# Kernel tuning notes

Measured on AMD Instinct MI355X. Metric: run time of the kernel, lower is better.

Reference implementation:

```python
import jax, jax.numpy as jnp
import numpy as np

B, T, D = 2, 1024, 768
H, HS = 12, 64          # n_head, head_size = n_embed // n_head
E, K = 8, 1             # num_experts, top-k (MoeLayer default k=1)
DF = 4 * D              # FFN hidden
EPS = 1e-5


def _ln(x, g, b):
    mu = jnp.mean(x, axis=-1, keepdims=True)
    var = jnp.mean(jnp.square(x - mu), axis=-1, keepdims=True)
    return (x - mu) * jax.lax.rsqrt(var + EPS) * g + b


def setup_inputs() -> dict:
    key = jax.random.key(0)
    ks = jax.random.split(key, 12)
    s = 0.02
    return {
        "x": jax.random.normal(ks[0], (B, T, D), dtype=jnp.float32),
        "ln1_g": jnp.ones((D,), jnp.float32),
        "ln1_b": jnp.zeros((D,), jnp.float32),
        "ln2_g": jnp.ones((D,), jnp.float32),
        "ln2_b": jnp.zeros((D,), jnp.float32),
        "Wq": jax.random.normal(ks[1], (H, D, HS), jnp.float32) * s,
        "Wk": jax.random.normal(ks[2], (H, D, HS), jnp.float32) * s,
        "Wv": jax.random.normal(ks[3], (H, D, HS), jnp.float32) * s,
        "Wp": jax.random.normal(ks[4], (D, D), jnp.float32) * s,
        "bp": jnp.zeros((D,), jnp.float32),
        "Wg": jax.random.normal(ks[5], (D, E), jnp.float32) * s,
        "W1": jax.random.normal(ks[6], (E, D, DF), jnp.float32) * s,
        "b1": jnp.zeros((E, DF), jnp.float32),
        "W2": jax.random.normal(ks[7], (E, DF, D), jnp.float32) * s,
        "b2": jnp.zeros((E, D), jnp.float32),
    }


def reference(x, ln1_g, ln1_b, ln2_g, ln2_b, Wq, Wk, Wv, Wp, bp, Wg, W1, b1, W2, b2):
    b, t, d = x.shape

    # ---- multi-head causal self-attention (per-head QKV, as in Head) ----
    h = _ln(x, ln1_g, ln1_b)
    q = jnp.einsum('btd,hds->bhts', h, Wq)
    k = jnp.einsum('btd,hds->bhts', h, Wk)
    v = jnp.einsum('btd,hds->bhts', h, Wv)
    # NOTE: original scales by C**-0.5 with C = n_embed (not head_size)
    scores = jnp.einsum('bhts,bhus->bhtu', q, k) * (d ** -0.5)
    causal = jnp.tril(jnp.ones((t, t), dtype=bool))
    scores = jnp.where(causal, scores, -jnp.inf)
    att = jax.nn.softmax(scores, axis=-1)
    out = jnp.einsum('bhtu,bhus->bhts', att, v)          # [B,H,T,HS]
    out = out.transpose(0, 2, 1, 3).reshape(b, t, d)     # concat heads
    x = x + out @ Wp + bp

    # ---- top-k MoE feed-forward (MoeLayer, k=1) ----
    h2 = _ln(x, ln2_g, ln2_b).reshape(-1, d)             # [N,D]
    gate_logits = h2 @ Wg                                # [N,E]
    w, sel = jax.lax.top_k(gate_logits, K)               # [N,K]
    w = jax.nn.softmax(w.astype(jnp.float32), axis=-1).astype(x.dtype)
    n = h2.shape[0]
    combine = jnp.zeros((n, Wg.shape[1]), x.dtype).at[
        jnp.arange(n)[:, None], sel].add(w)              # [N,E]
    hid = jax.nn.relu(jnp.einsum('nd,edf->enf', h2, W1) + b1[:, None, :])
    y = jnp.einsum('enf,efd->end', hid, W2) + b2[:, None, :]
    moe = jnp.einsum('ne,end->nd', combine, y)           # dense dispatch
    return x + moe.reshape(b, t, d)
```

## Files before the change

kernel.cpp:

```cpp
#include <hip/hip_runtime.h>
#include <math.h>

typedef __bf16 bf16;
typedef __bf16 bf16x8 __attribute__((ext_vector_type(8)));
typedef float f32x4 __attribute__((ext_vector_type(4)));

#define N_TOK 2048
#define DMODEL 768
#define NHEAD 12
#define TSEQ 1024
#define NEXP 8
#define DFF 3072

__device__ inline f32x4 mfma16(bf16x8 a, bf16x8 b, f32x4 c) {
    return __builtin_amdgcn_mfma_f32_16x16x32_bf16(a, b, c, 0, 0, 0);
}

__device__ inline f32x4 zero4() { f32x4 z = {0.f, 0.f, 0.f, 0.f}; return z; }

__device__ inline float block_sum(float v, float* red, int tid) {
#pragma unroll
    for (int off = 32; off > 0; off >>= 1) v += __shfl_down(v, off, 64);
    __syncthreads();
    if ((tid & 63) == 0) red[tid >> 6] = v;
    __syncthreads();
    return red[0] + red[1] + red[2] + red[3];
}

__global__ __launch_bounds__(256) void ln1_kernel(const float* __restrict__ x,
        const float* __restrict__ g, const float* __restrict__ b,
        bf16* __restrict__ hh, bf16* __restrict__ hl) {
    __shared__ float red[4];
    int row = blockIdx.x, tid = threadIdx.x;
    const float* xr = x + (size_t)row * DMODEL;
    float v[3];
#pragma unroll
    for (int i = 0; i < 3; i++) v[i] = xr[tid + i * 256];
    float s = block_sum(v[0] + v[1] + v[2], red, tid);
    float mu = s * (1.f / DMODEL);
    float q = 0.f;
#pragma unroll
    for (int i = 0; i < 3; i++) { float d = v[i] - mu; q += d * d; }
    q = block_sum(q, red, tid);
    float rstd = 1.0f / sqrtf(q * (1.f / DMODEL) + 1e-5f);
#pragma unroll
    for (int i = 0; i < 3; i++) {
        int d = tid + i * 256;
        float val = (v[i] - mu) * rstd * g[d] + b[d];
        bf16 hi = (bf16)val;
        hh[(size_t)row * DMODEL + d] = hi;
        hl[(size_t)row * DMODEL + d] = (bf16)(val - (float)hi);
    }
}

__device__ inline void gemm_step3(const bf16* lah, const bf16* lal,
                                  const bf16* lbh, const bf16* lbl,
                                  int wm, int wn, int row16, int quad,
                                  f32x4 acc[4][4]) {
    bf16x8 ah[4], al[4], bh[4], bl[4];
#pragma unroll
    for (int i = 0; i < 4; i++) {
        int ro = (wm * 64 + i * 16 + row16) * 40 + quad * 8;
        ah[i] = *(const bf16x8*)&lah[ro];
        al[i] = *(const bf16x8*)&lal[ro];
    }
#pragma unroll
    for (int i = 0; i < 4; i++) {
        int ro = (wn * 64 + i * 16 + row16) * 40 + quad * 8;
        bh[i] = *(const bf16x8*)&lbh[ro];
        bl[i] = *(const bf16x8*)&lbl[ro];
    }
#pragma unroll
    for (int mi = 0; mi < 4; mi++)
#pragma unroll
        for (int ni = 0; ni < 4; ni++) {
            acc[mi][ni] = mfma16(ah[mi], bh[ni], acc[mi][ni]);
            acc[mi][ni] = mfma16(ah[mi], bl[ni], acc[mi][ni]);
            acc[mi][ni] = mfma16(al[mi], bh[ni], acc[mi][ni]);
        }
}

__device__ inline void gemm_step1(const bf16* la, const bf16* lb, int wm, int wn,
                                  int row16, int quad, f32x4 acc[4][4]) {
    bf16x8 af[4], bfr[4];
#pragma unroll
    for (int i = 0; i < 4; i++)
        af[i] = *(const bf16x8*)&la[(wm * 64 + i * 16 + row16) * 40 + quad * 8];
#pragma unroll
    for (int i = 0; i < 4; i++)
        bfr[i] = *(const bf16x8*)&lb[(wn * 64 + i * 16 + row16) * 40 + quad * 8];
#pragma unroll
    for (int mi = 0; mi < 4; mi++)
#pragma unroll
        for (int ni = 0; ni < 4; ni++)
            acc[mi][ni] = mfma16(af[mi], bfr[ni], acc[mi][ni]);
}

__device__ inline void stage_A(bf16* la, const bf16* Abase, int lda, int k0, int tid) {
#pragma unroll
    for (int i = 0; i < 2; i++) {
        int chunk = tid + i * 256;
        int r = chunk >> 2, c = (chunk & 3) << 3;
        *(bf16x8*)&la[r * 40 + c] = *(const bf16x8*)&Abase[(size_t)r * lda + k0 + c];
    }
}

__global__ __launch_bounds__(256) void qkv_gemm(const bf16* __restrict__ hA_h,
        const bf16* __restrict__ hA_l,
        const float* __restrict__ Wq, const float* __restrict__ Wk,
        const float* __restrict__ Wv,
        bf16* __restrict__ qh, bf16* __restrict__ ql,
        bf16* __restrict__ kh, bf16* __restrict__ kl,
        bf16* __restrict__ vh, bf16* __restrict__ vl) {
    __shared__ alignas(16) bf16 lah[128 * 40];
    __shared__ alignas(16) bf16 lal[128 * 40];
    __shared__ alignas(16) bf16 lbh[128 * 40];
    __shared__ alignas(16) bf16 lbl[128 * 40];
    int tid = threadIdx.x;
    int m0 = blockIdx.y * 128;
    int nt = blockIdx.x;
    int sel = nt / 6;
    int n0 = (nt % 6) * 128;
    const float* W = (sel == 0) ? Wq : (sel == 1) ? Wk : Wv;
    bf16* obh = (sel == 0) ? qh : (sel == 1) ? kh : vh;
    bf16* obl = (sel == 0) ? ql : (sel == 1) ? kl : vl;
    int lane = tid & 63, w = tid >> 6, row16 = lane & 15, quad = lane >> 4;
    int wm = w >> 1, wn = w & 1;
    f32x4 acc[4][4];
#pragma unroll
    for (int mi = 0; mi < 4; mi++)
#pragma unroll
        for (int ni = 0; ni < 4; ni++) acc[mi][ni] = zero4();
    const bf16* Arow_h = hA_h + (size_t)m0 * DMODEL;
    const bf16* Arow_l = hA_l + (size_t)m0 * DMODEL;
    for (int k0 = 0; k0 < DMODEL; k0 += 32) {
        __syncthreads();
        stage_A(lah, Arow_h, DMODEL, k0, tid);
        stage_A(lal, Arow_l, DMODEL, k0, tid);
#pragma unroll
        for (int i = 0; i < 16; i++) {
            int idx = tid + (i << 8);
            int k = idx >> 7, n = idx & 127;
            int col = n0 + n;
            float val = W[((size_t)(col >> 6) * DMODEL + k0 + k) * 64 + (col & 63)];
            bf16 hi = (bf16)val;
            lbh[n * 40 + k] = hi;
            lbl[n * 40 + k] = (bf16)(val - (float)hi);
        }
        __syncthreads();
        gemm_step3(lah, lal, lbh, lbl, wm, wn, row16, quad, acc);
    }
#pragma unroll
    for (int mi = 0; mi < 4; mi++) {
        int rowl = wm * 64 + mi * 16 + quad * 4;
#pragma unroll
        for (int ni = 0; ni < 4; ni++) {
            int col = n0 + wn * 64 + ni * 16 + row16;
            int hhd = col >> 6, s = col & 63;
#pragma unroll
            for (int r = 0; r < 4; r++) {
                int gm = m0 + rowl + r;
                int bb = gm >> 10, t = gm & 1023;
                size_t oi = (((size_t)bb * NHEAD + hhd) * TSEQ + t) * 64 + s;
                float val = acc[mi][ni][r];
                bf16 hi = (bf16)val;
                obh[oi] = hi;
                obl[oi] = (bf16)(val - (float)hi);
            }
        }
    }
}

__global__ __launch_bounds__(256) void attn_kernel(const bf16* __restrict__ qhb,
        const bf16* __restrict__ qlb, const bf16* __restrict__ khb,
        const bf16* __restrict__ klb, const bf16* __restrict__ vhb,
        const bf16* __restrict__ vlb, bf16* __restrict__ aoh,
        bf16* __restrict__ aol) {
    __shared__ alignas(16) bf16 kt_h[64 * 72];
    __shared__ alignas(16) bf16 kt_l[64 * 72];
    __shared__ alignas(16) bf16 vt_h[64 * 72];
    __shared__ alignas(16) bf16 vt_l[64 * 72];
    __shared__ alignas(16) bf16 p_h[4][16 * 72];
    __shared__ alignas(16) bf16 p_l[4][16 * 72];
    int qt = blockIdx.x, bh = blockIdx.y;
    int b = bh / NHEAD, hh = bh % NHEAD;
    int tid = threadIdx.x, lane = tid & 63, w = tid >> 6;
    int row16 = lane & 15, quad = lane >> 4;
    const bf16* qph = qhb + (size_t)bh * TSEQ * 64;
    const bf16* qpl = qlb + (size_t)bh * TSEQ * 64;
    const bf16* kph = khb + (size_t)bh * TSEQ * 64;
    const bf16* kpl = klb + (size_t)bh * TSEQ * 64;
    const bf16* vph = vhb + (size_t)bh * TSEQ * 64;
    const bf16* vpl = vlb + (size_t)bh * TSEQ * 64;
    int qrow = qt * 64 + w * 16 + row16;
    bf16x8 aq_h[2], aq_l[2];
#pragma unroll
    for (int kk = 0; kk < 2; kk++) {
        aq_h[kk] = *(const bf16x8*)&qph[(size_t)qrow * 64 + kk * 32 + quad * 8];
        aq_l[kk] = *(const bf16x8*)&qpl[(size_t)qrow * 64 + kk * 32 + quad * 8];
    }
    f32x4 o[4];
    float m_i[4], l_i[4];
#pragma unroll
    for (int i = 0; i < 4; i++) { o[i] = zero4(); m_i[i] = -INFINITY; l_i[i] = 0.f; }
    const float sc = 0.03608439182435161f;
    for (int kt = 0; kt <= qt; kt++) {
        __syncthreads();
#pragma unroll
        for (int i = 0; i < 2; i++) {
            int chunk = tid + i * 256;
            int r = chunk >> 3, c = (chunk & 7) << 3;
            size_t gi = (size_t)(kt * 64 + r) * 64 + c;
            *(bf16x8*)&kt_h[r * 72 + c] = *(const bf16x8*)&kph[gi];
            *(bf16x8*)&kt_l[r * 72 + c] = *(const bf16x8*)&kpl[gi];
        }
#pragma unroll
        for (int i = 0; i < 16; i++) {
            int idx = tid + (i << 8);
            int tk = idx >> 6, s = idx & 63;
            size_t gi = (size_t)(kt * 64 + tk) * 64 + s;
            vt_h[s * 72 + tk] = vph[gi];
            vt_l[s * 72 + tk] = vpl[gi];
        }
        __syncthreads();
        f32x4 sacc[4];
#pragma unroll
        for (int ni = 0; ni < 4; ni++) {
            sacc[ni] = zero4();
#pragma unroll
            for (int kk = 0; kk < 2; kk++) {
                int ro = (ni * 16 + row16) * 72 + kk * 32 + quad * 8;
                bf16x8 bk_h = *(const bf16x8*)&kt_h[ro];
                bf16x8 bk_l = *(const bf16x8*)&kt_l[ro];
                sacc[ni] = mfma16(aq_h[kk], bk_h, sacc[ni]);
                sacc[ni] = mfma16(aq_h[kk], bk_l, sacc[ni]);
                sacc[ni] = mfma16(aq_l[kk], bk_h, sacc[ni]);
            }
        }
        float mrow[4];
#pragma unroll
        for (int r = 0; r < 4; r++) mrow[r] = -INFINITY;
        int tq_b = qt * 64 + w * 16 + quad * 4;
#pragma unroll
        for (int ni = 0; ni < 4; ni++) {
            int tkg = kt * 64 + ni * 16 + row16;
#pragma unroll
            for (int r = 0; r < 4; r++) {
                float sv = sacc[ni][r] * sc;
                if (tkg > tq_b + r) sv = -INFINITY;
                sacc[ni][r] = sv;
                mrow[r] = fmaxf(mrow[r], sv);
            }
        }
#pragma unroll
        for (int r = 0; r < 4; r++) {
#pragma unroll
            for (int off = 8; off > 0; off >>= 1)
                mrow[r] = fmaxf(mrow[r], __shfl_xor(mrow[r], off, 16));
        }
        float alpha[4], rsum[4];
#pragma unroll
        for (int r = 0; r < 4; r++) {
            float nm = fmaxf(m_i[r], mrow[r]);
            alpha[r] = __expf(m_i[r] - nm);
            m_i[r] = nm;
            rsum[r] = 0.f;
        }
#pragma unroll
        for (int ni = 0; ni < 4; ni++)
#pragma unroll
            for (int r = 0; r < 4; r++) {
                float p = __expf(sacc[ni][r] - m_i[r]);
                sacc[ni][r] = p;
                rsum[r] += p;
            }
#pragma unroll
        for (int r = 0; r < 4; r++) {
#pragma unroll
            for (int off = 8; off > 0; off >>= 1)
                rsum[r] += __shfl_xor(rsum[r], off, 16);
            l_i[r] = l_i[r] * alpha[r] + rsum[r];
        }
#pragma unroll
        for (int ni = 0; ni < 4; ni++)
#pragma unroll
            for (int r = 0; r < 4; r++) o[ni][r] *= alpha[r];
#pragma unroll
        for (int ni = 0; ni < 4; ni++)
#pragma unroll
            for (int r = 0; r < 4; r++) {
                float p = sacc[ni][r];
                bf16 hi = (bf16)p;
                int po = (quad * 4 + r) * 72 + ni * 16 + row16;
                p_h[w][po] = hi;
                p_l[w][po] = (bf16)(p - (float)hi);
            }
        __syncthreads();
        bf16x8 ap_h[2], ap_l[2];
#pragma unroll
        for (int kk = 0; kk < 2; kk++) {
            ap_h[kk] = *(const bf16x8*)&p_h[w][row16 * 72 + kk * 32 + quad * 8];
            ap_l[kk] = *(const bf16x8*)&p_l[w][row16 * 72 + kk * 32 + quad * 8];
        }
#pragma unroll
        for (int ni = 0; ni < 4; ni++)
#pragma unroll
            for (int kk = 0; kk < 2; kk++) {
                int ro = (ni * 16 + row16) * 72 + kk * 32 + quad * 8;
                bf16x8 bv_h = *(const bf16x8*)&vt_h[ro];
                bf16x8 bv_l = *(const bf16x8*)&vt_l[ro];
                o[ni] = mfma16(ap_h[kk], bv_h, o[ni]);
                o[ni] = mfma16(ap_h[kk], bv_l, o[ni]);
                o[ni] = mfma16(ap_l[kk], bv_h, o[ni]);
            }
    }
    int t = qt * 64 + w * 16 + quad * 4;
#pragma unroll
    for (int ni = 0; ni < 4; ni++) {
        int col = hh * 64 + ni * 16 + row16;
#pragma unroll
        for (int r = 0; r < 4; r++) {
            float val = o[ni][r] / l_i[r];
            size_t n = (size_t)b * TSEQ + t + r;
            bf16 hi = (bf16)val;
            aoh[n * DMODEL + col] = hi;
            aol[n * DMODEL + col] = (bf16)(val - (float)hi);
        }
    }
}

__global__ __launch_bounds__(256) void proj_gemm(const bf16* __restrict__ aInH,
        const bf16* __restrict__ aInL,
        const float* __restrict__ Wp, const float* __restrict__ bp,
        const float* __restrict__ x, float* __restrict__ x1) {
    __shared__ alignas(16) bf16 lah[128 * 40];
    __shared__ alignas(16) bf16 lal[128 * 40];
    __shared__ alignas(16) bf16 lbh[128 * 40];
    __shared__ alignas(16) bf16 lbl[128 * 40];
    int tid = threadIdx.x;
    int m0 = blockIdx.y * 128, n0 = blockIdx.x * 128;
    int lane = tid & 63, w = tid >> 6, row16 = lane & 15, quad = lane >> 4;
    int wm = w >> 1, wn = w & 1;
    f32x4 acc[4][4];
#pragma unroll
    for (int mi = 0; mi < 4; mi++)
#pragma unroll
        for (int ni = 0; ni < 4; ni++) acc[mi][ni] = zero4();
    const bf16* Arow_h = aInH + (size_t)m0 * DMODEL;
    const bf16* Arow_l = aInL + (size_t)m0 * DMODEL;
    for (int k0 = 0; k0 < DMODEL; k0 += 32) {
        __syncthreads();
        stage_A(lah, Arow_h, DMODEL, k0, tid);
        stage_A(lal, Arow_l, DMODEL, k0, tid);
#pragma unroll
        for (int i = 0; i < 16; i++) {
            int idx = tid + (i << 8);
            int kk = idx >> 7, n = idx & 127;
            float val = Wp[(size_t)(k0 + kk) * DMODEL + n0 + n];
            bf16 hi = (bf16)val;
            lbh[n * 40 + kk] = hi;
            lbl[n * 40 + kk] = (bf16)(val - (float)hi);
        }
        __syncthreads();
        gemm_step3(lah, lal, lbh, lbl, wm, wn, row16, quad, acc);
    }
#pragma unroll
    for (int mi = 0; mi < 4; mi++) {
        int rowl = wm * 64 + mi * 16 + quad * 4;
#pragma unroll
        for (int ni = 0; ni < 4; ni++) {
            int col = n0 + wn * 64 + ni * 16 + row16;
#pragma unroll
            for (int r = 0; r < 4; r++) {
                int gm = m0 + rowl + r;
                x1[(size_t)gm * DMODEL + col] =
                    acc[mi][ni][r] + bp[col] + x[(size_t)gm * DMODEL + col];
            }
        }
    }
}

__global__ __launch_bounds__(256) void ln2_gate_kernel(const float* __restrict__ x1,
        const float* __restrict__ g, const float* __restrict__ b,
        const float* __restrict__ Wg, bf16* __restrict__ h2,
        int* __restrict__ sel, int* __restrict__ counts) {
    __shared__ float red[4];
    __shared__ float glog[8];
    int row = blockIdx.x, tid = threadIdx.x;
    if (tid < 8) glog[tid] = 0.f;
    const float* xr = x1 + (size_t)row * DMODEL;
    float v[3];
#pragma unroll
    for (int i = 0; i < 3; i++) v[i] = xr[tid + i * 256];
    float s = block_sum(v[0] + v[1] + v[2], red, tid);
    float mu = s * (1.f / DMODEL);
    float qv = 0.f;
#pragma unroll
    for (int i = 0; i < 3; i++) { float d = v[i] - mu; qv += d * d; }
    qv = block_sum(qv, red, tid);
    float rstd = 1.0f / sqrtf(qv * (1.f / DMODEL) + 1e-5f);
    float ga[8];
#pragma unroll
    for (int e = 0; e < 8; e++) ga[e] = 0.f;
#pragma unroll
    for (int i = 0; i < 3; i++) {
        int d = tid + i * 256;
        float hv = (v[i] - mu) * rstd * g[d] + b[d];
        h2[(size_t)row * DMODEL + d] = (bf16)hv;
        const float* wgr = Wg + (size_t)d * NEXP;
#pragma unroll
        for (int e = 0; e < 8; e++) ga[e] += hv * wgr[e];
    }
#pragma unroll
    for (int e = 0; e < 8; e++)
#pragma unroll
        for (int off = 32; off > 0; off >>= 1) ga[e] += __shfl_down(ga[e], off, 64);
    if ((tid & 63) == 0)
#pragma unroll
        for (int e = 0; e < 8; e++) atomicAdd(&glog[e], ga[e]);
    __syncthreads();
    if (tid == 0) {
        float best = glog[0];
        int bi = 0;
#pragma unroll
        for (int e = 1; e < 8; e++)
            if (glog[e] > best) { best = glog[e]; bi = e; }
        sel[row] = bi;
        atomicAdd(&counts[bi], 1);
    }
}

__global__ void zero_kernel(int* __restrict__ p, int n) {
    int i = blockIdx.x * blockDim.x + threadIdx.x;
    if (i < n) p[i] = 0;
}
__global__ void scan_kernel(const int* __restrict__ counts, int* __restrict__ offsets) {
    if (threadIdx.x == 0) {
        int o = 0;
        for (int e = 0; e < NEXP; e++) { offsets[e] = o; o += counts[e]; }
    }
}
__global__ void scatter_kernel(const int* __restrict__ sel, const int* __restrict__ offsets,
                               int* __restrict__ cursor, int* __restrict__ perm) {
    int n = blockIdx.x * blockDim.x + threadIdx.x;
    if (n >= N_TOK) return;
    int e = sel[n];
    int pos = atomicAdd(&cursor[e], 1);
    perm[offsets[e] + pos] = n;
}

__global__ __launch_bounds__(256) void moe1_gemm(const bf16* __restrict__ h2,
        const float* __restrict__ W1, const float* __restrict__ b1,
        const int* __restrict__ counts, const int* __restrict__ offsets,
        const int* __restrict__ perm, bf16* __restrict__ hid) {
    int e = blockIdx.z;
    int cnt = counts[e];
    int rt = blockIdx.y;
    if (rt * 128 >= cnt) return;
    int off = offsets[e];
    int n0 = blockIdx.x * 128;
    const float* W = W1 + (size_t)e * DMODEL * DFF;
    __shared__ alignas(16) bf16 la[128 * 40];
    __shared__ alignas(16) bf16 lb[128 * 40];
    int tid = threadIdx.x;
    int lane = tid & 63, w = tid >> 6, row16 = lane & 15, quad = lane >> 4;
    int wm = w >> 1, wn = w & 1;
    int r_a = tid >> 2, c_a = (tid & 3) << 3;
    int tok0 = perm[off + min(rt * 128 + r_a, cnt - 1)];
    int tok1 = perm[off + min(rt * 128 + r_a + 64, cnt - 1)];
    f32x4 acc[4][4];
#pragma unroll
    for (int mi = 0; mi < 4; mi++)
#pragma unroll
        for (int ni = 0; ni < 4; ni++) acc[mi][ni] = zero4();
    for (int k0 = 0; k0 < DMODEL; k0 += 32) {
        __syncthreads();
        *(bf16x8*)&la[r_a * 40 + c_a] = *(const bf16x8*)&h2[(size_t)tok0 * DMODEL + k0 + c_a];
        *(bf16x8*)&la[(r_a + 64) * 40 + c_a] = *(const bf16x8*)&h2[(size_t)tok1 * DMODEL + k0 + c_a];
#pragma unroll
        for (int i = 0; i < 16; i++) {
            int idx = tid + (i << 8);
            int kk = idx >> 7, n = idx & 127;
            lb[n * 40 + kk] = (bf16)W[(size_t)(k0 + kk) * DFF + n0 + n];
        }
        __syncthreads();
        gemm_step1(la, lb, wm, wn, row16, quad, acc);
    }
#pragma unroll
    for (int mi = 0; mi < 4; mi++) {
        int rowl = wm * 64 + mi * 16 + quad * 4;
#pragma unroll
        for (int ni = 0; ni < 4; ni++) {
            int col = n0 + wn * 64 + ni * 16 + row16;
#pragma unroll
            for (int r = 0; r < 4; r++) {
                int lr = rowl + r;
                if (rt * 128 + lr < cnt) {
                    float val = acc[mi][ni][r] + b1[(size_t)e * DFF + col];
                    val = fmaxf(val, 0.f);
                    hid[(size_t)(off + rt * 128 + lr) * DFF + col] = (bf16)val;
                }
            }
        }
    }
}

__global__ __launch_bounds__(256) void moe2_gemm(const bf16* __restrict__ hid,
        const float* __restrict__ W2, const float* __restrict__ b2,
        const int* __restrict__ counts, const int* __restrict__ offsets,
        const int* __restrict__ perm, const float* __restrict__ x1,
        float* __restrict__ out) {
    int e = blockIdx.z;
    int cnt = counts[e];
    int rt = blockIdx.y;
    if (rt * 128 >= cnt) return;
    int off = offsets[e];
    int n0 = blockIdx.x * 128;
    const float* W = W2 + (size_t)e * DFF * DMODEL;
    __shared__ alignas(16) bf16 la[128 * 40];
    __shared__ alignas(16) bf16 lb[128 * 40];
    int tid = threadIdx.x;
    int lane = tid & 63, w = tid >> 6, row16 = lane & 15, quad = lane >> 4;
    int wm = w >> 1, wn = w & 1;
    int r_a = tid >> 2, c_a = (tid & 3) << 3;
    const bf16* arow0 = hid + (size_t)min(off + rt * 128 + r_a, N_TOK - 1) * DFF;
    const bf16* arow1 = hid + (size_t)min(off + rt * 128 + r_a + 64, N_TOK - 1) * DFF;
    f32x4 acc[4][4];
#pragma unroll
    for (int mi = 0; mi < 4; mi++)
#pragma unroll
        for (int ni = 0; ni < 4; ni++) acc[mi][ni] = zero4();
    for (int k0 = 0; k0 < DFF; k0 += 32) {
        __syncthreads();
        *(bf16x8*)&la[r_a * 40 + c_a] = *(const bf16x8*)&arow0[k0 + c_a];
        *(bf16x8*)&la[(r_a + 64) * 40 + c_a] = *(const bf16x8*)&arow1[k0 + c_a];
#pragma unroll
        for (int i = 0; i < 16; i++) {
            int idx = tid + (i << 8);
            int kk = idx >> 7, n = idx & 127;
            lb[n * 40 + kk] = (bf16)W[(size_t)(k0 + kk) * DMODEL + n0 + n];
        }
        __syncthreads();
        gemm_step1(la, lb, wm, wn, row16, quad, acc);
    }
#pragma unroll
    for (int mi = 0; mi < 4; mi++) {
        int rowl = wm * 64 + mi * 16 + quad * 4;
#pragma unroll
        for (int ni = 0; ni < 4; ni++) {
            int col = n0 + wn * 64 + ni * 16 + row16;
#pragma unroll
            for (int r = 0; r < 4; r++) {
                int lr = rowl + r;
                if (rt * 128 + lr < cnt) {
                    int n = perm[off + rt * 128 + lr];
                    out[(size_t)n * DMODEL + col] =
                        acc[mi][ni][r] + b2[(size_t)e * DMODEL + col] +
                        x1[(size_t)n * DMODEL + col];
                }
            }
        }
    }
}

extern "C" void kernel_launch(void* const* d_in, const int* in_sizes, int n_in,
                              void* d_out, int out_size, void* d_ws, size_t ws_size,
                              hipStream_t stream) {
    const float* x    = (const float*)d_in[0];
    const float* ln1g = (const float*)d_in[1];
    const float* ln1b = (const float*)d_in[2];
    const float* ln2g = (const float*)d_in[3];
    const float* ln2b = (const float*)d_in[4];
    const float* Wq   = (const float*)d_in[5];
    const float* Wk   = (const float*)d_in[6];
    const float* Wv   = (const float*)d_in[7];
    const float* Wp   = (const float*)d_in[8];
    const float* bp   = (const float*)d_in[9];
    const float* Wg   = (const float*)d_in[10];
    const float* W1   = (const float*)d_in[11];
    const float* b1   = (const float*)d_in[12];
    const float* W2   = (const float*)d_in[13];
    const float* b2   = (const float*)d_in[14];
    float* out = (float*)d_out;

    char* ws = (char*)d_ws;
    size_t off = 0;
    const size_t SZ = (size_t)N_TOK * DMODEL * 2;
    bf16* h1h = (bf16*)(ws + off); off += SZ;
    bf16* h1l = (bf16*)(ws + off); off += SZ;
    bf16* qh  = (bf16*)(ws + off); off += SZ;
    bf16* ql  = (bf16*)(ws + off); off += SZ;
    bf16* kh  = (bf16*)(ws + off); off += SZ;
    bf16* kl  = (bf16*)(ws + off); off += SZ;
    bf16* vh  = (bf16*)(ws + off); off += SZ;
    bf16* vl  = (bf16*)(ws + off); off += SZ;
    bf16* aoh = (bf16*)(ws + off); off += SZ;
    bf16* aol = (bf16*)(ws + off); off += SZ;
    float* x1 = (float*)(ws + off); off += (size_t)N_TOK * DMODEL * 4;
    bf16* h2  = (bf16*)(ws + off); off += SZ;
    bf16* hid = (bf16*)(ws + off); off += (size_t)N_TOK * DFF * 2;
    int* counts  = (int*)(ws + off); off += 8 * 4;
    int* cursor  = (int*)(ws + off); off += 8 * 4;
    int* offsets = (int*)(ws + off); off += 8 * 4;
    int* sel     = (int*)(ws + off); off += (size_t)N_TOK * 4;
    int* perm    = (int*)(ws + off); off += (size_t)N_TOK * 4;

    zero_kernel<<<1, 64, 0, stream>>>(counts, 16);
    ln1_kernel<<<N_TOK, 256, 0, stream>>>(x, ln1g, ln1b, h1h, h1l);
    qkv_gemm<<<dim3(18, 16), 256, 0, stream>>>(h1h, h1l, Wq, Wk, Wv, qh, ql, kh, kl, vh, vl);
    attn_kernel<<<dim3(16, 24), 256, 0, stream>>>(qh, ql, kh, kl, vh, vl, aoh, aol);
    proj_gemm<<<dim3(6, 16), 256, 0, stream>>>(aoh, aol, Wp, bp, x, x1);
    ln2_gate_kernel<<<N_TOK, 256, 0, stream>>>(x1, ln2g, ln2b, Wg, h2, sel, counts);
    scan_kernel<<<1, 64, 0, stream>>>(counts, offsets);
    scatter_kernel<<<8, 256, 0, stream>>>(sel, offsets, cursor, perm);
    moe1_gemm<<<dim3(24, 16, 8), 256, 0, stream>>>(h2, W1, b1, counts, offsets, perm, hid);
    moe2_gemm<<<dim3(6, 16, 8), 256, 0, stream>>>(hid, W2, b2, counts, offsets, perm, x1, out);
}
```

Baseline: 637.9 us.

## Double-buffer LDS tiles in GEMMs and split-K the second MoE GEMM

```diff
diff --git a/kernel.cpp b/kernel.cpp
--- a/kernel.cpp
+++ b/kernel.cpp
@@ -96,14 +96,7 @@
             acc[mi][ni] = mfma16(af[mi], bfr[ni], acc[mi][ni]);
 }
 
-__device__ inline void stage_A(bf16* la, const bf16* Abase, int lda, int k0, int tid) {
-#pragma unroll
-    for (int i = 0; i < 2; i++) {
-        int chunk = tid + i * 256;
-        int r = chunk >> 2, c = (chunk & 3) << 3;
-        *(bf16x8*)&la[r * 40 + c] = *(const bf16x8*)&Abase[(size_t)r * lda + k0 + c];
-    }
-}
+#define TILE_E (128 * 40)
 
 __global__ __launch_bounds__(256) void qkv_gemm(const bf16* __restrict__ hA_h,
         const bf16* __restrict__ hA_l,
@@ -112,10 +105,10 @@
         bf16* __restrict__ qh, bf16* __restrict__ ql,
         bf16* __restrict__ kh, bf16* __restrict__ kl,
         bf16* __restrict__ vh, bf16* __restrict__ vl) {
-    __shared__ alignas(16) bf16 lah[128 * 40];
-    __shared__ alignas(16) bf16 lal[128 * 40];
-    __shared__ alignas(16) bf16 lbh[128 * 40];
-    __shared__ alignas(16) bf16 lbl[128 * 40];
+    __shared__ alignas(16) bf16 lah[2 * TILE_E];
+    __shared__ alignas(16) bf16 lal[2 * TILE_E];
+    __shared__ alignas(16) bf16 lbh[2 * TILE_E];
+    __shared__ alignas(16) bf16 lbl[2 * TILE_E];
     int tid = threadIdx.x;
     int m0 = blockIdx.y * 128;
     int nt = blockIdx.x;
@@ -126,29 +119,62 @@
     bf16* obl = (sel == 0) ? ql : (sel == 1) ? kl : vl;
     int lane = tid & 63, w = tid >> 6, row16 = lane & 15, quad = lane >> 4;
     int wm = w >> 1, wn = w & 1;
+    int r_a = tid >> 2, c_a = (tid & 3) << 3;
+    int nW = tid & 127, kbase = tid >> 7;
+    size_t wcol = (size_t)((n0 + nW) >> 6) * DMODEL * 64 + ((n0 + nW) & 63);
     f32x4 acc[4][4];
 #pragma unroll
     for (int mi = 0; mi < 4; mi++)
 #pragma unroll
         for (int ni = 0; ni < 4; ni++) acc[mi][ni] = zero4();
-    const bf16* Arow_h = hA_h + (size_t)m0 * DMODEL;
-    const bf16* Arow_l = hA_l + (size_t)m0 * DMODEL;
-    for (int k0 = 0; k0 < DMODEL; k0 += 32) {
+    const bf16* Ah = hA_h + (size_t)m0 * DMODEL;
+    const bf16* Al = hA_l + (size_t)m0 * DMODEL;
+
+    bf16x8 rAh0, rAh1, rAl0, rAl1;
+    float wv[16];
+    rAh0 = *(const bf16x8*)&Ah[(size_t)r_a * DMODEL + c_a];
+    rAh1 = *(const bf16x8*)&Ah[(size_t)(r_a + 64) * DMODEL + c_a];
+    rAl0 = *(const bf16x8*)&Al[(size_t)r_a * DMODEL + c_a];
+    rAl1 = *(const bf16x8*)&Al[(size_t)(r_a + 64) * DMODEL + c_a];
+#pragma unroll
+    for (int i = 0; i < 16; i++) wv[i] = W[wcol + (size_t)(kbase + 2 * i) * 64];
+    *(bf16x8*)&lah[r_a * 40 + c_a] = rAh0;
+    *(bf16x8*)&lah[(r_a + 64) * 40 + c_a] = rAh1;
+    *(bf16x8*)&lal[r_a * 40 + c_a] = rAl0;
+    *(bf16x8*)&lal[(r_a + 64) * 40 + c_a] = rAl1;
+#pragma unroll
+    for (int i = 0; i < 16; i++) {
+        bf16 hi = (bf16)wv[i];
+        lbh[nW * 40 + kbase + 2 * i] = hi;
+        lbl[nW * 40 + kbase + 2 * i] = (bf16)(wv[i] - (float)hi);
+    }
+    const int nk = DMODEL / 32;
+    for (int ki = 0; ki < nk; ki++) {
         __syncthreads();
-        stage_A(lah, Arow_h, DMODEL, k0, tid);
-        stage_A(lal, Arow_l, DMODEL, k0, tid);
-#pragma unroll
-        for (int i = 0; i < 16; i++) {
-            int idx = tid + (i << 8);
-            int k = idx >> 7, n = idx & 127;
-            int col = n0 + n;
-            float val = W[((size_t)(col >> 6) * DMODEL + k0 + k) * 64 + (col & 63)];
-            bf16 hi = (bf16)val;
-            lbh[n * 40 + k] = hi;
-            lbl[n * 40 + k] = (bf16)(val - (float)hi);
-        }
-        __syncthreads();
-        gemm_step3(lah, lal, lbh, lbl, wm, wn, row16, quad, acc);
+        int cur = (ki & 1) * TILE_E, nxt = ((ki + 1) & 1) * TILE_E;
+        if (ki + 1 < nk) {
+            int k0 = (ki + 1) * 32;
+            rAh0 = *(const bf16x8*)&Ah[(size_t)r_a * DMODEL + k0 + c_a];
+            rAh1 = *(const bf16x8*)&Ah[(size_t)(r_a + 64) * DMODEL + k0 + c_a];
+            rAl0 = *(const bf16x8*)&Al[(size_t)r_a * DMODEL + k0 + c_a];
+            rAl1 = *(const bf16x8*)&Al[(size_t)(r_a + 64) * DMODEL + k0 + c_a];
+#pragma unroll
+            for (int i = 0; i < 16; i++)
+                wv[i] = W[wcol + (size_t)(k0 + kbase + 2 * i) * 64];
+        }
+        gemm_step3(lah + cur, lal + cur, lbh + cur, lbl + cur, wm, wn, row16, quad, acc);
+        if (ki + 1 < nk) {
+            *(bf16x8*)&lah[nxt + r_a * 40 + c_a] = rAh0;
+            *(bf16x8*)&lah[nxt + (r_a + 64) * 40 + c_a] = rAh1;
+            *(bf16x8*)&lal[nxt + r_a * 40 + c_a] = rAl0;
+            *(bf16x8*)&lal[nxt + (r_a + 64) * 40 + c_a] = rAl1;
+#pragma unroll
+            for (int i = 0; i < 16; i++) {
+                bf16 hi = (bf16)wv[i];
+                lbh[nxt + nW * 40 + kbase + 2 * i] = hi;
+                lbl[nxt + nW * 40 + kbase + 2 * i] = (bf16)(wv[i] - (float)hi);
+            }
+        }
     }
 #pragma unroll
     for (int mi = 0; mi < 4; mi++) {
@@ -333,36 +359,69 @@
         const bf16* __restrict__ aInL,
         const float* __restrict__ Wp, const float* __restrict__ bp,
         const float* __restrict__ x, float* __restrict__ x1) {
-    __shared__ alignas(16) bf16 lah[128 * 40];
-    __shared__ alignas(16) bf16 lal[128 * 40];
-    __shared__ alignas(16) bf16 lbh[128 * 40];
-    __shared__ alignas(16) bf16 lbl[128 * 40];
+    __shared__ alignas(16) bf16 lah[2 * TILE_E];
+    __shared__ alignas(16) bf16 lal[2 * TILE_E];
+    __shared__ alignas(16) bf16 lbh[2 * TILE_E];
+    __shared__ alignas(16) bf16 lbl[2 * TILE_E];
     int tid = threadIdx.x;
     int m0 = blockIdx.y * 128, n0 = blockIdx.x * 128;
     int lane = tid & 63, w = tid >> 6, row16 = lane & 15, quad = lane >> 4;
     int wm = w >> 1, wn = w & 1;
+    int r_a = tid >> 2, c_a = (tid & 3) << 3;
+    int nW = tid & 127, kbase = tid >> 7;
     f32x4 acc[4][4];
 #pragma unroll
     for (int mi = 0; mi < 4; mi++)
 #pragma unroll
         for (int ni = 0; ni < 4; ni++) acc[mi][ni] = zero4();
-    const bf16* Arow_h = aInH + (size_t)m0 * DMODEL;
-    const bf16* Arow_l = aInL + (size_t)m0 * DMODEL;
-    for (int k0 = 0; k0 < DMODEL; k0 += 32) {
+    const bf16* Ah = aInH + (size_t)m0 * DMODEL;
+    const bf16* Al = aInL + (size_t)m0 * DMODEL;
+    bf16x8 rAh0, rAh1, rAl0, rAl1;
+    float wv[16];
+    rAh0 = *(const bf16x8*)&Ah[(size_t)r_a * DMODEL + c_a];
+    rAh1 = *(const bf16x8*)&Ah[(size_t)(r_a + 64) * DMODEL + c_a];
+    rAl0 = *(const bf16x8*)&Al[(size_t)r_a * DMODEL + c_a];
+    rAl1 = *(const bf16x8*)&Al[(size_t)(r_a + 64) * DMODEL + c_a];
+#pragma unroll
+    for (int i = 0; i < 16; i++)
+        wv[i] = Wp[(size_t)(kbase + 2 * i) * DMODEL + n0 + nW];
+    *(bf16x8*)&lah[r_a * 40 + c_a] = rAh0;
+    *(bf16x8*)&lah[(r_a + 64) * 40 + c_a] = rAh1;
+    *(bf16x8*)&lal[r_a * 40 + c_a] = rAl0;
+    *(bf16x8*)&lal[(r_a + 64) * 40 + c_a] = rAl1;
+#pragma unroll
+    for (int i = 0; i < 16; i++) {
+        bf16 hi = (bf16)wv[i];
+        lbh[nW * 40 + kbase + 2 * i] = hi;
+        lbl[nW * 40 + kbase + 2 * i] = (bf16)(wv[i] - (float)hi);
+    }
+    const int nk = DMODEL / 32;
+    for (int ki = 0; ki < nk; ki++) {
         __syncthreads();
-        stage_A(lah, Arow_h, DMODEL, k0, tid);
-        stage_A(lal, Arow_l, DMODEL, k0, tid);
-#pragma unroll
-        for (int i = 0; i < 16; i++) {
-            int idx = tid + (i << 8);
-            int kk = idx >> 7, n = idx & 127;
-            float val = Wp[(size_t)(k0 + kk) * DMODEL + n0 + n];
-            bf16 hi = (bf16)val;
-            lbh[n * 40 + kk] = hi;
-            lbl[n * 40 + kk] = (bf16)(val - (float)hi);
-        }
-        __syncthreads();
-        gemm_step3(lah, lal, lbh, lbl, wm, wn, row16, quad, acc);
+        int cur = (ki & 1) * TILE_E, nxt = ((ki + 1) & 1) * TILE_E;
+        if (ki + 1 < nk) {
+            int k0 = (ki + 1) * 32;
+            rAh0 = *(const bf16x8*)&Ah[(size_t)r_a * DMODEL + k0 + c_a];
+            rAh1 = *(const bf16x8*)&Ah[(size_t)(r_a + 64) * DMODEL + k0 + c_a];
+            rAl0 = *(const bf16x8*)&Al[(size_t)r_a * DMODEL + k0 + c_a];
+            rAl1 = *(const bf16x8*)&Al[(size_t)(r_a + 64) * DMODEL + k0 + c_a];
+#pragma unroll
+            for (int i = 0; i < 16; i++)
+                wv[i] = Wp[(size_t)(k0 + kbase + 2 * i) * DMODEL + n0 + nW];
+        }
+        gemm_step3(lah + cur, lal + cur, lbh + cur, lbl + cur, wm, wn, row16, quad, acc);
+        if (ki + 1 < nk) {
+            *(bf16x8*)&lah[nxt + r_a * 40 + c_a] = rAh0;
+            *(bf16x8*)&lah[nxt + (r_a + 64) * 40 + c_a] = rAh1;
+            *(bf16x8*)&lal[nxt + r_a * 40 + c_a] = rAl0;
+            *(bf16x8*)&lal[nxt + (r_a + 64) * 40 + c_a] = rAl1;
+#pragma unroll
+            for (int i = 0; i < 16; i++) {
+                bf16 hi = (bf16)wv[i];
+                lbh[nxt + nW * 40 + kbase + 2 * i] = hi;
+                lbl[nxt + nW * 40 + kbase + 2 * i] = (bf16)(wv[i] - (float)hi);
+            }
+        }
     }
 #pragma unroll
     for (int mi = 0; mi < 4; mi++) {
@@ -433,6 +492,11 @@
 __global__ void zero_kernel(int* __restrict__ p, int n) {
     int i = blockIdx.x * blockDim.x + threadIdx.x;
     if (i < n) p[i] = 0;
+}
+__global__ void zero_out_kernel(float* __restrict__ p) {
+    int i = blockIdx.x * blockDim.x + threadIdx.x;
+    f32x4 z = zero4();
+    *(f32x4*)&p[i * 4] = z;
 }
 __global__ void scan_kernel(const int* __restrict__ counts, int* __restrict__ offsets) {
     if (threadIdx.x == 0) {
@@ -460,31 +524,52 @@
     int off = offsets[e];
     int n0 = blockIdx.x * 128;
     const float* W = W1 + (size_t)e * DMODEL * DFF;
-    __shared__ alignas(16) bf16 la[128 * 40];
-    __shared__ alignas(16) bf16 lb[128 * 40];
+    __shared__ alignas(16) bf16 la[2 * TILE_E];
+    __shared__ alignas(16) bf16 lb[2 * TILE_E];
     int tid = threadIdx.x;
     int lane = tid & 63, w = tid >> 6, row16 = lane & 15, quad = lane >> 4;
     int wm = w >> 1, wn = w & 1;
     int r_a = tid >> 2, c_a = (tid & 3) << 3;
+    int nW = tid & 127, kbase = tid >> 7;
     int tok0 = perm[off + min(rt * 128 + r_a, cnt - 1)];
     int tok1 = perm[off + min(rt * 128 + r_a + 64, cnt - 1)];
+    const bf16* a0 = h2 + (size_t)tok0 * DMODEL;
+    const bf16* a1 = h2 + (size_t)tok1 * DMODEL;
     f32x4 acc[4][4];
 #pragma unroll
     for (int mi = 0; mi < 4; mi++)
 #pragma unroll
         for (int ni = 0; ni < 4; ni++) acc[mi][ni] = zero4();
-    for (int k0 = 0; k0 < DMODEL; k0 += 32) {
+    bf16x8 rA0, rA1;
+    float wv[16];
+    rA0 = *(const bf16x8*)&a0[c_a];
+    rA1 = *(const bf16x8*)&a1[c_a];
+#pragma unroll
+    for (int i = 0; i < 16; i++)
+        wv[i] = W[(size_t)(kbase + 2 * i) * DFF + n0 + nW];
+    *(bf16x8*)&la[r_a * 40 + c_a] = rA0;
+    *(bf16x8*)&la[(r_a + 64) * 40 + c_a] = rA1;
+#pragma unroll
+    for (int i = 0; i < 16; i++) lb[nW * 40 + kbase + 2 * i] = (bf16)wv[i];
+    const int nk = DMODEL / 32;
+    for (int ki = 0; ki < nk; ki++) {
         __syncthreads();
-        *(bf16x8*)&la[r_a * 40 + c_a] = *(const bf16x8*)&h2[(size_t)tok0 * DMODEL + k0 + c_a];
-        *(bf16x8*)&la[(r_a + 64) * 40 + c_a] = *(const bf16x8*)&h2[(size_t)tok1 * DMODEL + k0 + c_a];
-#pragma unroll
-        for (int i = 0; i < 16; i++) {
-            int idx = tid + (i << 8);
-            int kk = idx >> 7, n = idx & 127;
-            lb[n * 40 + kk] = (bf16)W[(size_t)(k0 + kk) * DFF + n0 + n];
-        }
-        __syncthreads();
-        gemm_step1(la, lb, wm, wn, row16, quad, acc);
+        int cur = (ki & 1) * TILE_E, nxt = ((ki + 1) & 1) * TILE_E;
+        if (ki + 1 < nk) {
+            int k0 = (ki + 1) * 32;
+            rA0 = *(const bf16x8*)&a0[k0 + c_a];
+            rA1 = *(const bf16x8*)&a1[k0 + c_a];
+#pragma unroll
+            for (int i = 0; i < 16; i++)
+                wv[i] = W[(size_t)(k0 + kbase + 2 * i) * DFF + n0 + nW];
+        }
+        gemm_step1(la + cur, lb + cur, wm, wn, row16, quad, acc);
+        if (ki + 1 < nk) {
+            *(bf16x8*)&la[nxt + r_a * 40 + c_a] = rA0;
+            *(bf16x8*)&la[nxt + (r_a + 64) * 40 + c_a] = rA1;
+#pragma unroll
+            for (int i = 0; i < 16; i++) lb[nxt + nW * 40 + kbase + 2 * i] = (bf16)wv[i];
+        }
     }
 #pragma unroll
     for (int mi = 0; mi < 4; mi++) {
@@ -510,38 +595,59 @@
         const int* __restrict__ counts, const int* __restrict__ offsets,
         const int* __restrict__ perm, const float* __restrict__ x1,
         float* __restrict__ out) {
-    int e = blockIdx.z;
+    int ez = blockIdx.z;
+    int e = ez >> 1, ks = ez & 1;
     int cnt = counts[e];
     int rt = blockIdx.y;
     if (rt * 128 >= cnt) return;
     int off = offsets[e];
     int n0 = blockIdx.x * 128;
     const float* W = W2 + (size_t)e * DFF * DMODEL;
-    __shared__ alignas(16) bf16 la[128 * 40];
-    __shared__ alignas(16) bf16 lb[128 * 40];
+    __shared__ alignas(16) bf16 la[2 * TILE_E];
+    __shared__ alignas(16) bf16 lb[2 * TILE_E];
     int tid = threadIdx.x;
     int lane = tid & 63, w = tid >> 6, row16 = lane & 15, quad = lane >> 4;
     int wm = w >> 1, wn = w & 1;
     int r_a = tid >> 2, c_a = (tid & 3) << 3;
-    const bf16* arow0 = hid + (size_t)min(off + rt * 128 + r_a, N_TOK - 1) * DFF;
-    const bf16* arow1 = hid + (size_t)min(off + rt * 128 + r_a + 64, N_TOK - 1) * DFF;
+    int nW = tid & 127, kbase = tid >> 7;
+    const bf16* a0 = hid + (size_t)min(off + rt * 128 + r_a, N_TOK - 1) * DFF;
+    const bf16* a1 = hid + (size_t)min(off + rt * 128 + r_a + 64, N_TOK - 1) * DFF;
     f32x4 acc[4][4];
 #pragma unroll
     for (int mi = 0; mi < 4; mi++)
 #pragma unroll
         for (int ni = 0; ni < 4; ni++) acc[mi][ni] = zero4();
-    for (int k0 = 0; k0 < DFF; k0 += 32) {
+    const int kst = ks * (DFF / 2);
+    bf16x8 rA0, rA1;
+    float wv[16];
+    rA0 = *(const bf16x8*)&a0[kst + c_a];
+    rA1 = *(const bf16x8*)&a1[kst + c_a];
+#pragma unroll
+    for (int i = 0; i < 16; i++)
+        wv[i] = W[(size_t)(kst + kbase + 2 * i) * DMODEL + n0 + nW];
+    *(bf16x8*)&la[r_a * 40 + c_a] = rA0;
+    *(bf16x8*)&la[(r_a + 64) * 40 + c_a] = rA1;
+#pragma unroll
+    for (int i = 0; i < 16; i++) lb[nW * 40 + kbase + 2 * i] = (bf16)wv[i];
+    const int nk = (DFF / 2) / 32;
+    for (int ki = 0; ki < nk; ki++) {
         __syncthreads();
-        *(bf16x8*)&la[r_a * 40 + c_a] = *(const bf16x8*)&arow0[k0 + c_a];
-        *(bf16x8*)&la[(r_a + 64) * 40 + c_a] = *(const bf16x8*)&arow1[k0 + c_a];
-#pragma unroll
-        for (int i = 0; i < 16; i++) {
-            int idx = tid + (i << 8);
-            int kk = idx >> 7, n = idx & 127;
-            lb[n * 40 + kk] = (bf16)W[(size_t)(k0 + kk) * DMODEL + n0 + n];
-        }
-        __syncthreads();
-        gemm_step1(la, lb, wm, wn, row16, quad, acc);
+        int cur = (ki & 1) * TILE_E, nxt = ((ki + 1) & 1) * TILE_E;
+        if (ki + 1 < nk) {
+            int k0 = kst + (ki + 1) * 32;
+            rA0 = *(const bf16x8*)&a0[k0 + c_a];
+            rA1 = *(const bf16x8*)&a1[k0 + c_a];
+#pragma unroll
+            for (int i = 0; i < 16; i++)
+                wv[i] = W[(size_t)(k0 + kbase + 2 * i) * DMODEL + n0 + nW];
+        }
+        gemm_step1(la + cur, lb + cur, wm, wn, row16, quad, acc);
+        if (ki + 1 < nk) {
+            *(bf16x8*)&la[nxt + r_a * 40 + c_a] = rA0;
+            *(bf16x8*)&la[nxt + (r_a + 64) * 40 + c_a] = rA1;
+#pragma unroll
+            for (int i = 0; i < 16; i++) lb[nxt + nW * 40 + kbase + 2 * i] = (bf16)wv[i];
+        }
     }
 #pragma unroll
     for (int mi = 0; mi < 4; mi++) {
@@ -554,9 +660,10 @@
                 int lr = rowl + r;
                 if (rt * 128 + lr < cnt) {
                     int n = perm[off + rt * 128 + lr];
-                    out[(size_t)n * DMODEL + col] =
-                        acc[mi][ni][r] + b2[(size_t)e * DMODEL + col] +
-                        x1[(size_t)n * DMODEL + col];
+                    float val = acc[mi][ni][r];
+                    if (ks == 0)
+                        val += b2[(size_t)e * DMODEL + col] + x1[(size_t)n * DMODEL + col];
+                    atomicAdd(&out[(size_t)n * DMODEL + col], val);
                 }
             }
         }
@@ -606,6 +713,7 @@
     int* perm    = (int*)(ws + off); off += (size_t)N_TOK * 4;
 
     zero_kernel<<<1, 64, 0, stream>>>(counts, 16);
+    zero_out_kernel<<<N_TOK * DMODEL / 4 / 256, 256, 0, stream>>>(out);
     ln1_kernel<<<N_TOK, 256, 0, stream>>>(x, ln1g, ln1b, h1h, h1l);
     qkv_gemm<<<dim3(18, 16), 256, 0, stream>>>(h1h, h1l, Wq, Wk, Wv, qh, ql, kh, kl, vh, vl);
     attn_kernel<<<dim3(16, 24), 256, 0, stream>>>(qh, ql, kh, kl, vh, vl, aoh, aol);
@@ -614,5 +722,5 @@
     scan_kernel<<<1, 64, 0, stream>>>(counts, offsets);
     scatter_kernel<<<8, 256, 0, stream>>>(sel, offsets, cursor, perm);
     moe1_gemm<<<dim3(24, 16, 8), 256, 0, stream>>>(h2, W1, b1, counts, offsets, perm, hid);
-    moe2_gemm<<<dim3(6, 16, 8), 256, 0, stream>>>(hid, W2, b2, counts, offsets, perm, x1, out);
-}
+    moe2_gemm<<<dim3(6, 16, 16), 256, 0, stream>>>(hid, W2, b2, counts, offsets, perm, x1, out);
+}
```

New measurement: 540.0 us. -15.3%, faster.
